# Kernel tuning notes

Hardware: AMD Instinct MI355X
Metric: run time of the kernel (lower is better)

Reference implementation:

```python
import jax, jax.numpy as jnp
import numpy as np
import math

EMBED = 1024
FF = 4096
HEADS = 16
HEAD = EMBED // HEADS
EPS = 1e-5


def new_gelu(x):
    c = math.sqrt(2.0 / math.pi)
    return 0.5 * x * (1.0 + jnp.tanh(c * (x + 0.044715 * x ** 3)))


def layer_norm(x, g, b):
    mu = jnp.mean(x, axis=-1, keepdims=True)
    var = jnp.var(x, axis=-1, keepdims=True)
    return (x - mu) * jax.lax.rsqrt(var + EPS) * g + b


def setup_inputs() -> dict:
    key = jax.random.key(0)
    ks = jax.random.split(key, 16)
    s = 0.02
    d = {
        'x': jax.random.normal(ks[0], (2, 2048, EMBED), jnp.float32),
        'Wq': jax.random.normal(ks[1], (EMBED, EMBED)) * s,
        'bq': jnp.zeros((EMBED,)),
        'Wk': jax.random.normal(ks[2], (EMBED, EMBED)) * s,
        'bk': jnp.zeros((EMBED,)),
        'Wv': jax.random.normal(ks[3], (EMBED, EMBED)) * s,
        'bv': jnp.zeros((EMBED,)),
        'Wp': jax.random.normal(ks[4], (EMBED, EMBED)) * s,
        'bp': jnp.zeros((EMBED,)),
        'W1': jax.random.normal(ks[5], (EMBED, FF)) * s,
        'b1': jnp.zeros((FF,)),
        'W2': jax.random.normal(ks[6], (FF, EMBED)) * s,
        'b2': jnp.zeros((EMBED,)),
        'g1': jnp.ones((EMBED,)), 'be1': jnp.zeros((EMBED,)),
        'g2': jnp.ones((EMBED,)), 'be2': jnp.zeros((EMBED,)),
    }
    return d


def reference(x, Wq, bq, Wk, bk, Wv, bv, Wp, bp, W1, b1, W2, b2, g1, be1, g2, be2):
    B, S, D = x.shape
    h = layer_norm(x, g1, be1)
    # project and split heads: [B,S,D] -> [B,H,S,Hd]
    def heads(y):
        return y.reshape(B, S, HEADS, HEAD).transpose(0, 2, 1, 3)
    Q = heads(h @ Wq + bq)
    K = heads(h @ Wk + bk)
    V = heads(h @ Wv + bv)
    att = jnp.einsum('bhqd,bhkd->bhqk', Q, K) / math.sqrt(HEAD)
    att = jax.nn.softmax(att, axis=-1)
    out = jnp.einsum('bhqk,bhkd->bhqd', att, V)
    out = out.transpose(0, 2, 1, 3).reshape(B, S, D)
    x = x + (out @ Wp + bp)  # dropout p=0 / eval -> identity
    h2 = layer_norm(x, g2, be2)
    x = x + (new_gelu(h2 @ W1 + b1) @ W2 + b2)
    return x
```

## Files before the change

### kernel.cpp

```cpp
#include <hip/hip_runtime.h>
#include <cstdint>


typedef __attribute__((ext_vector_type(8))) short short8;
typedef __attribute__((ext_vector_type(4))) float f32x4;

__device__ __forceinline__ float bf2f(unsigned short u) {
    union { unsigned int i; float f; } v; v.i = ((unsigned int)u) << 16; return v.f;
}
__device__ __forceinline__ unsigned short f2bf(float f) {
    union { float f; unsigned int i; } v; v.f = f;
    unsigned int u = v.i;
    u += 0x7fff + ((u >> 16) & 1);
    return (unsigned short)(u >> 16);
}
__device__ __forceinline__ float gelu_f(float x) {
    float u = 0.7978845608028654f * (x + 0.044715f * x * x * x);
    float t = 1.f - 2.f / (__expf(2.f * u) + 1.f);
    return 0.5f * x * (1.f + t);
}
__device__ __forceinline__ void async16(const unsigned short* gp, unsigned short* lp) {
    __builtin_amdgcn_global_load_lds(
        (__attribute__((address_space(1))) void*)(gp),
        (__attribute__((address_space(3))) void*)(lp),
        16, 0, 0);
}

__device__ __forceinline__ void ln_dev(
    const float* __restrict__ x, const float* __restrict__ g,
    const float* __restrict__ b, unsigned short* __restrict__ o,
    int row, float* red)
{
    const int tid = threadIdx.x;
    const float4 v = ((const float4*)(x + (size_t)row * 1024))[tid];
    float f0 = v.x, f1 = v.y, f2 = v.z, f3 = v.w;
    float sum = f0 + f1 + f2 + f3;
    float sq  = f0 * f0 + f1 * f1 + f2 * f2 + f3 * f3;
    for (int off = 1; off < 64; off <<= 1) {
        sum += __shfl_xor(sum, off);
        sq  += __shfl_xor(sq,  off);
    }
    int wv = tid >> 6, ln = tid & 63;
    if (ln == 0) { red[wv] = sum; red[4 + wv] = sq; }
    __syncthreads();
    sum = red[0] + red[1] + red[2] + red[3];
    sq  = red[4] + red[5] + red[6] + red[7];
    float mu  = sum * (1.0f / 1024.0f);
    float var = sq  * (1.0f / 1024.0f) - mu * mu;
    float rsd = rsqrtf(fmaxf(var, 0.f) + 1e-5f);
    const float4 gg = ((const float4*)g)[tid];
    const float4 bb = ((const float4*)b)[tid];
    unsigned short* orow = o + (size_t)row * 1024;
    orow[4 * tid + 0] = f2bf((f0 - mu) * rsd * gg.x + bb.x);
    orow[4 * tid + 1] = f2bf((f1 - mu) * rsd * gg.y + bb.y);
    orow[4 * tid + 2] = f2bf((f2 - mu) * rsd * gg.z + bb.z);
    orow[4 * tid + 3] = f2bf((f3 - mu) * rsd * gg.w + bb.w);
}

__device__ __forceinline__ void transpose_dev(
    const float* __restrict__ in, unsigned short* __restrict__ out,
    int R, int C, int inStride, int bx, int by, unsigned short* tile )
{
    const int tx = threadIdx.x & 15, ty = threadIdx.x >> 4;
    const int c0 = bx * 64, r0 = by * 64;
#pragma unroll
    for (int i = 0; i < 4; ++i) {
        int r = ty + 16 * i;
        float4 v = *(const float4*)(in + (size_t)(r0 + r) * inStride + c0 + tx * 4);
        tile[r * 70 + tx * 4 + 0] = f2bf(v.x);
        tile[r * 70 + tx * 4 + 1] = f2bf(v.y);
        tile[r * 70 + tx * 4 + 2] = f2bf(v.z);
        tile[r * 70 + tx * 4 + 3] = f2bf(v.w);
    }
    __syncthreads();
#pragma unroll
    for (int i = 0; i < 4; ++i) {
        int c = ty * 4 + i;
        ushort4 o;
        o.x = tile[(tx * 4 + 0) * 70 + c];
        o.y = tile[(tx * 4 + 1) * 70 + c];
        o.z = tile[(tx * 4 + 2) * 70 + c];
        o.w = tile[(tx * 4 + 3) * 70 + c];
        *(ushort4*)(out + (size_t)(c0 + c) * R + r0 + tx * 4) = o;
    }
}

__global__ __launch_bounds__(256) void ln_k(
    const float* __restrict__ x, const float* __restrict__ g,
    const float* __restrict__ b, unsigned short* __restrict__ o)
{
    __shared__ float red[8];
    ln_dev(x, g, b, o, blockIdx.x, red);
}
__global__ __launch_bounds__(256) void transpose_f2b(
    const float* __restrict__ in, unsigned short* __restrict__ out,
    int R, int C, int inStride)
{
    __shared__ unsigned short tile[64 * 70];
    transpose_dev(in, out, R, C, inStride, blockIdx.x, blockIdx.y, tile);
}
__global__ __launch_bounds__(256) void bcat_k(
    const float* __restrict__ a, const float* __restrict__ b,
    const float* __restrict__ c, float* __restrict__ dst)
{
    int i = blockIdx.x * 256 + threadIdx.x;
    float v = (i < 1024) ? a[i] : (i < 2048) ? b[i - 1024] : c[i - 2048];
    dst[i] = v;
}

__global__ __launch_bounds__(256) void prep1_k(
    const float* __restrict__ x,
    const float* __restrict__ g1, const float* __restrict__ be1,
    const float* __restrict__ Wq, const float* __restrict__ Wk,
    const float* __restrict__ Wv,
    const float* __restrict__ bq, const float* __restrict__ bk,
    const float* __restrict__ bv,
    unsigned short* __restrict__ hb,
    unsigned short* __restrict__ WTqkv,
    float* __restrict__ bcat)
{
    __shared__ unsigned short smem[64 * 70];
    const int b = blockIdx.x;
    if (b < 4096) {
        ln_dev(x, g1, be1, hb, b, (float*)smem);
    } else if (b < 4096 + 768) {
        int t = b - 4096;
        int w = t >> 8;
        int tt = t & 255;
        const float* W = (w == 0) ? Wq : (w == 1) ? Wk : Wv;
        transpose_dev(W, WTqkv + (size_t)w * 1024 * 1024,
                      1024, 1024, 1024, tt & 15, tt >> 4, smem);
    } else {
        int i = (b - 4096 - 768) * 256 + threadIdx.x;
        float v = (i < 1024) ? bq[i] : (i < 2048) ? bk[i - 1024] : bv[i - 2048];
        bcat[i] = v;
    }
}

__global__ __launch_bounds__(256) void prep2_k(
    const float* __restrict__ x1,
    const float* __restrict__ g2, const float* __restrict__ be2,
    const float* __restrict__ W1, const float* __restrict__ W2,
    unsigned short* __restrict__ h2,
    unsigned short* __restrict__ WT1,
    unsigned short* __restrict__ WT2)
{
    __shared__ unsigned short smem[64 * 70];
    const int b = blockIdx.x;
    if (b < 4096) {
        ln_dev(x1, g2, be2, h2, b, (float*)smem);
    } else if (b < 4096 + 1024) {
        int t = b - 4096;
        transpose_dev(W1, WT1, 1024, 4096, 4096, t & 63, t >> 6, smem);
    } else {
        int t = b - 4096 - 1024;
        transpose_dev(W2, WT2, 4096, 1024, 1024, t & 15, t >> 4, smem);
    }
}

__global__ __launch_bounds__(256) void vt_k(
    const unsigned short* __restrict__ src, int stride,
    unsigned short* __restrict__ Vt)
{
    __shared__ unsigned short tile[64][70];
    const int tx = threadIdx.x & 15, ty = threadIdx.x >> 4;
    const int t0 = blockIdx.x * 64;
    const int bh = blockIdx.y;
    const int bo = (bh >> 4) * 2048;
    const int ho = (bh & 15) * 64;
    const unsigned short* s = src + (size_t)bo * stride + ho;
#pragma unroll
    for (int i = 0; i < 4; ++i) {
        int r = ty + 16 * i;
        ushort4 v = *(const ushort4*)(s + (size_t)(t0 + r) * stride + tx * 4);
        tile[r][tx * 4 + 0] = v.x;
        tile[r][tx * 4 + 1] = v.y;
        tile[r][tx * 4 + 2] = v.z;
        tile[r][tx * 4 + 3] = v.w;
    }
    __syncthreads();
    unsigned short* dst = Vt + (size_t)bh * 64 * 2048;
#pragma unroll
    for (int i = 0; i < 4; ++i) {
        int d = ty * 4 + i;
#pragma unroll
        for (int c = 0; c < 4; ++c) {
            int t = tx * 4 + c;
            int sg = (t & 15) * 4 + (t >> 4);
            dst[(size_t)d * 2048 + t0 + sg] = tile[t][d];
        }
    }
}

__global__ __launch_bounds__(256, 2) void gemm_bt(
    const unsigned short* __restrict__ A,
    const unsigned short* __restrict__ Bt,
    const float* __restrict__ bias,
    const float* __restrict__ res,
    void* __restrict__ C,
    int M, int N, int K, int ldb, int dogelu, int out32)
{
    __shared__ unsigned short sA[2 * 128 * 32];
    __shared__ unsigned short sB[2 * 128 * 32];
    const int tid  = threadIdx.x;
    const int wave = tid >> 6;
    const int lane = tid & 63;
    const int quad = lane >> 4;
    const int l15  = lane & 15;
    const int bm = blockIdx.y * 128;
    const int bn = blockIdx.x * 128;
    const int wM = (wave >> 1) * 64;
    const int wN = (wave & 1) * 64;

    f32x4 acc[4][4];
#pragma unroll
    for (int i = 0; i < 4; ++i)
#pragma unroll
        for (int j = 0; j < 4; ++j)
            acc[i][j] = (f32x4){0.f, 0.f, 0.f, 0.f};

    const int rowS = tid >> 2;
    const int kcS  = (tid & 3) * 8;
    const unsigned short* gA  = A  + (size_t)(bm + rowS) * K + kcS;
    const unsigned short* gA2 = gA + (size_t)64 * K;
    const unsigned short* gB  = Bt + (size_t)(bn + rowS) * ldb + kcS;
    const unsigned short* gB2 = gB + (size_t)64 * ldb;
    unsigned short* lA  = sA + tid * 8;
    unsigned short* lA2 = lA + 64 * 32;
    unsigned short* lB  = sB + tid * 8;
    unsigned short* lB2 = lB + 64 * 32;

    for (int k0 = 0; k0 < K; k0 += 64) {
        __syncthreads();
        async16(gA + k0,       lA);
        async16(gA2 + k0,      lA2);
        async16(gA + k0 + 32,  lA + 4096);
        async16(gA2 + k0 + 32, lA2 + 4096);
        async16(gB + k0,       lB);
        async16(gB2 + k0,      lB2);
        async16(gB + k0 + 32,  lB + 4096);
        async16(gB2 + k0 + 32, lB2 + 4096);
        __syncthreads();

#pragma unroll
        for (int p = 0; p < 2; ++p) {
            short8 aF[4], bF[4];
#pragma unroll
            for (int mi = 0; mi < 4; ++mi)
                aF[mi] = *(const short8*)(sA + p * 4096 + (wM + mi * 16 + l15) * 32 + quad * 8);
#pragma unroll
            for (int ni = 0; ni < 4; ++ni)
                bF[ni] = *(const short8*)(sB + p * 4096 + (wN + ni * 16 + l15) * 32 + quad * 8);
#pragma unroll
            for (int mi = 0; mi < 4; ++mi)
#pragma unroll
                for (int ni = 0; ni < 4; ++ni)
                    acc[mi][ni] = __builtin_amdgcn_mfma_f32_16x16x32_bf16(
                        aF[mi], bF[ni], acc[mi][ni], 0, 0, 0);
        }
    }

#pragma unroll
    for (int ni = 0; ni < 4; ++ni) {
        int col = bn + wN + ni * 16 + l15;
        float bv = bias ? bias[col] : 0.f;
#pragma unroll
        for (int mi = 0; mi < 4; ++mi) {
            int row = bm + wM + mi * 16 + quad * 4;
#pragma unroll
            for (int r = 0; r < 4; ++r) {
                float v = acc[mi][ni][r] + bv;
                if (dogelu) v = gelu_f(v);
                size_t idx = (size_t)(row + r) * N + col;
                if (res) v += res[idx];
                if (out32) ((float*)C)[idx] = v;
                else       ((unsigned short*)C)[idx] = f2bf(v);
            }
        }
    }
}

__global__ __launch_bounds__(256, 2) void gemm_bt64(
    const unsigned short* __restrict__ A,
    const unsigned short* __restrict__ Bt,
    const float* __restrict__ bias,
    const float* __restrict__ res,
    void* __restrict__ C,
    int M, int N, int K, int ldb, int dogelu, int out32)
{
    __shared__ unsigned short sA[2 * 128 * 32];
    __shared__ unsigned short sB[2 * 64 * 32];
    const int tid  = threadIdx.x;
    const int wave = tid >> 6;
    const int lane = tid & 63;
    const int quad = lane >> 4;
    const int l15  = lane & 15;
    const int bm = blockIdx.y * 128;
    const int bn = blockIdx.x * 64;
    const int wM = wave * 32;

    f32x4 acc[2][4];
#pragma unroll
    for (int i = 0; i < 2; ++i)
#pragma unroll
        for (int j = 0; j < 4; ++j)
            acc[i][j] = (f32x4){0.f, 0.f, 0.f, 0.f};

    const int rowS = tid >> 2;
    const int kcS  = (tid & 3) * 8;
    const unsigned short* gA  = A  + (size_t)(bm + rowS) * K + kcS;
    const unsigned short* gA2 = gA + (size_t)64 * K;
    const unsigned short* gB  = Bt + (size_t)(bn + rowS) * ldb + kcS;
    unsigned short* lA  = sA + tid * 8;
    unsigned short* lA2 = lA + 64 * 32;
    unsigned short* lB  = sB + tid * 8;

    for (int k0 = 0; k0 < K; k0 += 64) {
        __syncthreads();
        async16(gA + k0,       lA);
        async16(gA2 + k0,      lA2);
        async16(gA + k0 + 32,  lA + 4096);
        async16(gA2 + k0 + 32, lA2 + 4096);
        async16(gB + k0,       lB);
        async16(gB + k0 + 32,  lB + 2048);
        __syncthreads();

#pragma unroll
        for (int p = 0; p < 2; ++p) {
            short8 aF[2], bF[4];
#pragma unroll
            for (int mi = 0; mi < 2; ++mi)
                aF[mi] = *(const short8*)(sA + p * 4096 + (wM + mi * 16 + l15) * 32 + quad * 8);
#pragma unroll
            for (int ni = 0; ni < 4; ++ni)
                bF[ni] = *(const short8*)(sB + p * 2048 + (ni * 16 + l15) * 32 + quad * 8);
#pragma unroll
            for (int mi = 0; mi < 2; ++mi)
#pragma unroll
                for (int ni = 0; ni < 4; ++ni)
                    acc[mi][ni] = __builtin_amdgcn_mfma_f32_16x16x32_bf16(
                        aF[mi], bF[ni], acc[mi][ni], 0, 0, 0);
        }
    }

#pragma unroll
    for (int ni = 0; ni < 4; ++ni) {
        int col = bn + ni * 16 + l15;
        float bv = bias ? bias[col] : 0.f;
#pragma unroll
        for (int mi = 0; mi < 2; ++mi) {
            int row = bm + wM + mi * 16 + quad * 4;
#pragma unroll
            for (int r = 0; r < 4; ++r) {
                float v = acc[mi][ni][r] + bv;
                if (dogelu) v = gelu_f(v);
                size_t idx = (size_t)(row + r) * N + col;
                if (res) v += res[idx];
                if (out32) ((float*)C)[idx] = v;
                else       ((unsigned short*)C)[idx] = f2bf(v);
            }
        }
    }
}

__global__ __launch_bounds__(256, 1) void attn_k(
    const unsigned short* __restrict__ Q,
    const unsigned short* __restrict__ K,
    const unsigned short* __restrict__ Vt,
    unsigned short* __restrict__ O, int qs)
{
    __shared__ unsigned short sK[2][64 * 88];
    __shared__ unsigned short sV[2][64 * 88];
    __shared__ unsigned short sP[4][64 * 88];

    const int tid  = threadIdx.x;
    const int wave = tid >> 6;
    const int lane = tid & 63;
    const int quad = lane >> 4;
    const int l15  = lane & 15;
    const int qb = blockIdx.x * 256;
    const int bh = blockIdx.y;
    const int bo = (bh >> 4) * 2048;
    const int ho = (bh & 15) * 64;

    const unsigned short* Qb  = Q  + (size_t)bo * qs + ho;
    const unsigned short* Kb  = K  + (size_t)bo * qs + ho;
    const unsigned short* Vtb = Vt + (size_t)bh * 64 * 2048;
    unsigned short* sPw = sP[wave];

    short8 qF[2][4];
#pragma unroll
    for (int ks = 0; ks < 2; ++ks)
#pragma unroll
        for (int mi = 0; mi < 4; ++mi)
            qF[ks][mi] = *(const short8*)(Qb +
                (size_t)(qb + wave * 64 + mi * 16 + l15) * qs + ks * 32 + quad * 8);

    short8 onesF;
#pragma unroll
    for (int j = 0; j < 8; ++j) onesF[j] = (short)0x3F80;

    f32x4 accO[4][4];
    f32x4 accL[4];
#pragma unroll
    for (int mi = 0; mi < 4; ++mi) {
        accL[mi] = (f32x4){0.f, 0.f, 0.f, 0.f};
#pragma unroll
        for (int nd = 0; nd < 4; ++nd) accO[mi][nd] = (f32x4){0.f, 0.f, 0.f, 0.f};
    }

    const int rowS = tid >> 3;
    const int dcS  = (tid & 7) * 8;

    short8 kr[2], vr[2];
#pragma unroll
    for (int r = 0; r < 2; ++r) {
        kr[r] = *(const short8*)(Kb + (size_t)(r * 32 + rowS) * qs + dcS);
        vr[r] = *(const short8*)(Vtb + (size_t)(r * 32 + rowS) * 2048 + dcS);
    }
#pragma unroll
    for (int r = 0; r < 2; ++r) {
        *(short8*)(&sK[0][(r * 32 + rowS) * 88 + dcS]) = kr[r];
        *(short8*)(&sV[0][(r * 32 + rowS) * 88 + dcS]) = vr[r];
    }
#pragma unroll
    for (int r = 0; r < 2; ++r) {
        kr[r] = *(const short8*)(Kb + (size_t)(64 + r * 32 + rowS) * qs + dcS);
        vr[r] = *(const short8*)(Vtb + (size_t)(r * 32 + rowS) * 2048 + 64 + dcS);
    }

    for (int kt = 0; kt < 2048; kt += 64) {
        const int buf = (kt >> 6) & 1;
        __syncthreads();

        short8 bK[2][4];
#pragma unroll
        for (int ks = 0; ks < 2; ++ks)
#pragma unroll
            for (int ni = 0; ni < 4; ++ni)
                bK[ks][ni] = *(const short8*)(&sK[buf][(ni * 16 + l15) * 88 + ks * 32 + quad * 8]);

#pragma unroll
        for (int mi = 0; mi < 4; ++mi) {
            f32x4 s0 = (f32x4){0.f, 0.f, 0.f, 0.f};
            f32x4 s1 = s0, s2 = s0, s3 = s0;
#pragma unroll
            for (int ks = 0; ks < 2; ++ks) {
                s0 = __builtin_amdgcn_mfma_f32_16x16x32_bf16(qF[ks][mi], bK[ks][0], s0, 0, 0, 0);
                s1 = __builtin_amdgcn_mfma_f32_16x16x32_bf16(qF[ks][mi], bK[ks][1], s1, 0, 0, 0);
                s2 = __builtin_amdgcn_mfma_f32_16x16x32_bf16(qF[ks][mi], bK[ks][2], s2, 0, 0, 0);
                s3 = __builtin_amdgcn_mfma_f32_16x16x32_bf16(qF[ks][mi], bK[ks][3], s3, 0, 0, 0);
            }
#pragma unroll
            for (int r = 0; r < 4; ++r) {
                float p0 = __expf(s0[r] * 0.125f);
                float p1 = __expf(s1[r] * 0.125f);
                float p2 = __expf(s2[r] * 0.125f);
                float p3 = __expf(s3[r] * 0.125f);
                unsigned int w0, w1;
                asm("v_cvt_pk_bf16_f32 %0, %1, %2" : "=v"(w0) : "v"(p0), "v"(p1));
                asm("v_cvt_pk_bf16_f32 %0, %1, %2" : "=v"(w1) : "v"(p2), "v"(p3));
                uint2 w; w.x = w0; w.y = w1;
                *(uint2*)(&sPw[(mi * 16 + quad * 4 + r) * 88 + l15 * 4]) = w;
            }
        }

        if (kt + 64 < 2048) {
            const int nb = buf ^ 1;
#pragma unroll
            for (int r = 0; r < 2; ++r) {
                *(short8*)(&sK[nb][(r * 32 + rowS) * 88 + dcS]) = kr[r];
                *(short8*)(&sV[nb][(r * 32 + rowS) * 88 + dcS]) = vr[r];
            }
            if (kt + 128 < 2048) {
#pragma unroll
                for (int r = 0; r < 2; ++r) {
                    kr[r] = *(const short8*)(Kb + (size_t)(kt + 128 + r * 32 + rowS) * qs + dcS);
                    vr[r] = *(const short8*)(Vtb + (size_t)(r * 32 + rowS) * 2048 + kt + 128 + dcS);
                }
            }
        }

        short8 bV[2][4];
#pragma unroll
        for (int ks = 0; ks < 2; ++ks)
#pragma unroll
            for (int nd = 0; nd < 4; ++nd)
                bV[ks][nd] = *(const short8*)(&sV[buf][(nd * 16 + l15) * 88 + ks * 32 + quad * 8]);

        __builtin_amdgcn_s_setprio(1);
#pragma unroll
        for (int mi = 0; mi < 4; ++mi) {
            short8 aP0 = *(const short8*)(&sPw[(mi * 16 + l15) * 88 + quad * 8]);
            short8 aP1 = *(const short8*)(&sPw[(mi * 16 + l15) * 88 + 32 + quad * 8]);
#pragma unroll
            for (int nd = 0; nd < 4; ++nd) {
                accO[mi][nd] = __builtin_amdgcn_mfma_f32_16x16x32_bf16(
                    aP0, bV[0][nd], accO[mi][nd], 0, 0, 0);
                accO[mi][nd] = __builtin_amdgcn_mfma_f32_16x16x32_bf16(
                    aP1, bV[1][nd], accO[mi][nd], 0, 0, 0);
            }
            accL[mi] = __builtin_amdgcn_mfma_f32_16x16x32_bf16(aP0, onesF, accL[mi], 0, 0, 0);
            accL[mi] = __builtin_amdgcn_mfma_f32_16x16x32_bf16(aP1, onesF, accL[mi], 0, 0, 0);
        }
        __builtin_amdgcn_s_setprio(0);
    }

#pragma unroll
    for (int mi = 0; mi < 4; ++mi)
#pragma unroll
        for (int r = 0; r < 4; ++r) {
            int row = qb + wave * 64 + mi * 16 + quad * 4 + r;
            float inv = 1.f / accL[mi][r];
#pragma unroll
            for (int nd = 0; nd < 4; ++nd)
                O[(size_t)(bo + row) * 1024 + ho + nd * 16 + l15] =
                    f2bf(accO[mi][nd][r] * inv);
        }
}

extern "C" void kernel_launch(void* const* d_in, const int* in_sizes, int n_in,
                              void* d_out, int out_size, void* d_ws, size_t ws_size,
                              hipStream_t stream)
{
    (void)in_sizes; (void)n_in; (void)out_size;
    const float* x   = (const float*)d_in[0];
    const float* Wq  = (const float*)d_in[1];
    const float* bq  = (const float*)d_in[2];
    const float* Wk  = (const float*)d_in[3];
    const float* bk  = (const float*)d_in[4];
    const float* Wv  = (const float*)d_in[5];
    const float* bv  = (const float*)d_in[6];
    const float* Wp  = (const float*)d_in[7];
    const float* bp  = (const float*)d_in[8];
    const float* W1  = (const float*)d_in[9];
    const float* b1  = (const float*)d_in[10];
    const float* W2  = (const float*)d_in[11];
    const float* b2  = (const float*)d_in[12];
    const float* g1  = (const float*)d_in[13];
    const float* be1 = (const float*)d_in[14];
    const float* g2  = (const float*)d_in[15];
    const float* be2 = (const float*)d_in[16];
    float* out = (float*)d_out;

    char* ws = (char*)d_ws;
    char* dob = (char*)d_out;
    const size_t MB = 1024 * 1024;

    if (ws_size >= 40 * MB) {
        unsigned short* hb    = (unsigned short*)dob;
        unsigned short* WTqkv = (unsigned short*)(dob + 8 * MB);
        float*          bcat  = (float*)(dob + 14 * MB);
        unsigned short* QKV   = (unsigned short*)ws;
        unsigned short* att   = (unsigned short*)(ws + 24 * MB);
        unsigned short* Vt    = (unsigned short*)(ws + 32 * MB);
        unsigned short* WTp   = (unsigned short*)(ws + 32 * MB);
        unsigned short* h2    = (unsigned short*)ws;
        unsigned short* WT1   = (unsigned short*)(ws + 8 * MB);
        unsigned short* WT2   = (unsigned short*)(ws + 16 * MB);
        unsigned short* act   = (unsigned short*)(ws + 24 * MB);

        prep1_k<<<4096 + 768 + 12, 256, 0, stream>>>(
            x, g1, be1, Wq, Wk, Wv, bq, bk, bv, hb, WTqkv, bcat);
        gemm_bt<<<dim3(24, 32), 256, 0, stream>>>(hb, WTqkv, bcat, nullptr, QKV,
                                                  4096, 3072, 1024, 1024, 0, 0);
        vt_k<<<dim3(32, 32), 256, 0, stream>>>(QKV + 2048, 3072, Vt);
        attn_k<<<dim3(8, 32), 256, 0, stream>>>(QKV, QKV + 1024, Vt, att, 3072);
        transpose_f2b<<<dim3(16, 16), 256, 0, stream>>>(Wp, WTp, 1024, 1024, 1024);
        gemm_bt64<<<dim3(16, 32), 256, 0, stream>>>(att, WTp, bp, x, out,
                                                    4096, 1024, 1024, 1024, 0, 1);
        prep2_k<<<4096 + 2048, 256, 0, stream>>>(out, g2, be2, W1, W2, h2, WT1, WT2);
        for (int c = 0; c < 2; ++c) {
            gemm_bt<<<dim3(16, 32), 256, 0, stream>>>(h2, WT1 + (size_t)c * 2048 * 1024,
                                                      b1 + c * 2048, nullptr, act,
                                                      4096, 2048, 1024, 1024, 1, 0);
            gemm_bt64<<<dim3(16, 32), 256, 0, stream>>>(act, WT2 + (size_t)c * 2048,
                                                        c == 0 ? b2 : nullptr, out, out,
                                                        4096, 1024, 2048, 4096, 0, 1);
        }
    } else {
        unsigned short* Qw  = (unsigned short*)(ws);
        unsigned short* Kw  = (unsigned short*)(ws + 8 * MB);
        unsigned short* Vw  = (unsigned short*)(ws + 16 * MB);
        unsigned short* hb  = (unsigned short*)dob;
        unsigned short* WTq = (unsigned short*)(dob + 8 * MB);
        unsigned short* VtF = (unsigned short*)(dob + 8 * MB);
        unsigned short* att = Qw;
        unsigned short* WTb = Kw;
        unsigned short* h2  = Vw;
        unsigned short* act = Qw;

        ln_k<<<4096, 256, 0, stream>>>(x, g1, be1, hb);
        transpose_f2b<<<dim3(16, 16), 256, 0, stream>>>(Wq, WTq, 1024, 1024, 1024);
        gemm_bt<<<dim3(8, 32), 256, 0, stream>>>(hb, WTq, bq, nullptr, Qw, 4096, 1024, 1024, 1024, 0, 0);
        transpose_f2b<<<dim3(16, 16), 256, 0, stream>>>(Wk, WTq, 1024, 1024, 1024);
        gemm_bt<<<dim3(8, 32), 256, 0, stream>>>(hb, WTq, bk, nullptr, Kw, 4096, 1024, 1024, 1024, 0, 0);
        transpose_f2b<<<dim3(16, 16), 256, 0, stream>>>(Wv, WTq, 1024, 1024, 1024);
        gemm_bt<<<dim3(8, 32), 256, 0, stream>>>(hb, WTq, bv, nullptr, Vw, 4096, 1024, 1024, 1024, 0, 0);
        vt_k<<<dim3(32, 32), 256, 0, stream>>>(Vw, 1024, VtF);
        attn_k<<<dim3(8, 32), 256, 0, stream>>>(Qw, Kw, VtF, att, 1024);
        transpose_f2b<<<dim3(16, 16), 256, 0, stream>>>(Wp, WTb, 1024, 1024, 1024);
        gemm_bt64<<<dim3(16, 32), 256, 0, stream>>>(att, WTb, bp, x, out, 4096, 1024, 1024, 1024, 0, 1);
        ln_k<<<4096, 256, 0, stream>>>(out, g2, be2, h2);
        for (int c = 0; c < 4; ++c) {
            transpose_f2b<<<dim3(16, 16), 256, 0, stream>>>(W1 + c * 1024, WTb, 1024, 1024, 4096);
            gemm_bt64<<<dim3(16, 32), 256, 0, stream>>>(h2, WTb, b1 + c * 1024, nullptr, act,
                                                        4096, 1024, 1024, 1024, 1, 0);
            unsigned short* WT2c = WTb + 1024 * 1024;
            transpose_f2b<<<dim3(16, 16), 256, 0, stream>>>(W2 + (size_t)c * 1024 * 1024, WT2c,
                                                            1024, 1024, 1024);
            gemm_bt64<<<dim3(16, 32), 256, 0, stream>>>(act, WT2c, c == 0 ? b2 : nullptr,
                                                        out, out, 4096, 1024, 1024, 1024, 0, 1);
        }
    }
}
```

Measured before the change: 399.3 us.

## Split attention keys across wave pairs, fold softmax scale into Wq, vectorize V transpose

Attention now runs 8 waves per block: each group of four waves shares a query tile, and the two halves split the QK^T key columns and the PV reduction dimension. Partial outputs are then combined through shared memory. The 1/sqrt(d)*log2(e) scale is folded into Wq and bq at transpose time, so the softmax uses exp2 directly with no per-element multiply. The V transpose kernel writes ushort4 vectors, and gemm_bt's launch bound rises to 3 blocks per SM. The attention kernel adds an extra barrier per tile and a final cross-wave reduction, and occupancy depends on the larger shared-memory footprint.

```diff
diff --git a/kernel.cpp b/kernel.cpp
--- a/kernel.cpp
+++ b/kernel.cpp
@@ -4,6 +4,8 @@
 
 typedef __attribute__((ext_vector_type(8))) short short8;
 typedef __attribute__((ext_vector_type(4))) float f32x4;
+
+#define QSCL 0.18033688011112042f
 
 __device__ __forceinline__ float bf2f(unsigned short u) {
     union { unsigned int i; float f; } v; v.i = ((unsigned int)u) << 16; return v.f;
@@ -59,7 +61,8 @@
 
 __device__ __forceinline__ void transpose_dev(
     const float* __restrict__ in, unsigned short* __restrict__ out,
-    int R, int C, int inStride, int bx, int by, unsigned short* tile )
+    int R, int C, int inStride, int bx, int by, unsigned short* tile ,
+    float scale)
 {
     const int tx = threadIdx.x & 15, ty = threadIdx.x >> 4;
     const int c0 = bx * 64, r0 = by * 64;
@@ -67,10 +70,10 @@
     for (int i = 0; i < 4; ++i) {
         int r = ty + 16 * i;
         float4 v = *(const float4*)(in + (size_t)(r0 + r) * inStride + c0 + tx * 4);
-        tile[r * 70 + tx * 4 + 0] = f2bf(v.x);
-        tile[r * 70 + tx * 4 + 1] = f2bf(v.y);
-        tile[r * 70 + tx * 4 + 2] = f2bf(v.z);
-        tile[r * 70 + tx * 4 + 3] = f2bf(v.w);
+        tile[r * 70 + tx * 4 + 0] = f2bf(v.x * scale);
+        tile[r * 70 + tx * 4 + 1] = f2bf(v.y * scale);
+        tile[r * 70 + tx * 4 + 2] = f2bf(v.z * scale);
+        tile[r * 70 + tx * 4 + 3] = f2bf(v.w * scale);
     }
     __syncthreads();
 #pragma unroll
@@ -94,18 +97,10 @@
 }
 __global__ __launch_bounds__(256) void transpose_f2b(
     const float* __restrict__ in, unsigned short* __restrict__ out,
-    int R, int C, int inStride)
+    int R, int C, int inStride, float scale)
 {
     __shared__ unsigned short tile[64 * 70];
-    transpose_dev(in, out, R, C, inStride, blockIdx.x, blockIdx.y, tile);
-}
-__global__ __launch_bounds__(256) void bcat_k(
-    const float* __restrict__ a, const float* __restrict__ b,
-    const float* __restrict__ c, float* __restrict__ dst)
-{
-    int i = blockIdx.x * 256 + threadIdx.x;
-    float v = (i < 1024) ? a[i] : (i < 2048) ? b[i - 1024] : c[i - 2048];
-    dst[i] = v;
+    transpose_dev(in, out, R, C, inStride, blockIdx.x, blockIdx.y, tile, scale);
 }
 
 __global__ __launch_bounds__(256) void prep1_k(
@@ -129,10 +124,11 @@
         int tt = t & 255;
         const float* W = (w == 0) ? Wq : (w == 1) ? Wk : Wv;
         transpose_dev(W, WTqkv + (size_t)w * 1024 * 1024,
-                      1024, 1024, 1024, tt & 15, tt >> 4, smem);
+                      1024, 1024, 1024, tt & 15, tt >> 4, smem,
+                      (w == 0) ? QSCL : 1.f);
     } else {
         int i = (b - 4096 - 768) * 256 + threadIdx.x;
-        float v = (i < 1024) ? bq[i] : (i < 2048) ? bk[i - 1024] : bv[i - 2048];
+        float v = (i < 1024) ? bq[i] * QSCL : (i < 2048) ? bk[i - 1024] : bv[i - 2048];
         bcat[i] = v;
     }
 }
@@ -151,10 +147,10 @@
         ln_dev(x1, g2, be2, h2, b, (float*)smem);
     } else if (b < 4096 + 1024) {
         int t = b - 4096;
-        transpose_dev(W1, WT1, 1024, 4096, 4096, t & 63, t >> 6, smem);
+        transpose_dev(W1, WT1, 1024, 4096, 4096, t & 63, t >> 6, smem, 1.f);
     } else {
         int t = b - 4096 - 1024;
-        transpose_dev(W2, WT2, 4096, 1024, 1024, t & 15, t >> 4, smem);
+        transpose_dev(W2, WT2, 4096, 1024, 1024, t & 15, t >> 4, smem, 1.f);
     }
 }
 
@@ -183,22 +179,23 @@
 #pragma unroll
     for (int i = 0; i < 4; ++i) {
         int d = ty * 4 + i;
-#pragma unroll
-        for (int c = 0; c < 4; ++c) {
-            int t = tx * 4 + c;
-            int sg = (t & 15) * 4 + (t >> 4);
-            dst[(size_t)d * 2048 + t0 + sg] = tile[t][d];
-        }
-    }
-}
-
-__global__ __launch_bounds__(256, 2) void gemm_bt(
+        int u = tx;
+        ushort4 o;
+        o.x = tile[u +  0][d];
+        o.y = tile[u + 16][d];
+        o.z = tile[u + 32][d];
+        o.w = tile[u + 48][d];
+        *(ushort4*)(dst + (size_t)d * 2048 + t0 + u * 4) = o;
+    }
+}
+
+__global__ __launch_bounds__(256, 3) void gemm_bt(
     const unsigned short* __restrict__ A,
     const unsigned short* __restrict__ Bt,
     const float* __restrict__ bias,
     const float* __restrict__ res,
     void* __restrict__ C,
-    int M, int N, int K, int ldb, int dogelu, int out32)
+    int M, int N, int K, int ldb, int dogelu, int out32, float bscale)
 {
     __shared__ unsigned short sA[2 * 128 * 32];
     __shared__ unsigned short sB[2 * 128 * 32];
@@ -263,7 +260,7 @@
 #pragma unroll
     for (int ni = 0; ni < 4; ++ni) {
         int col = bn + wN + ni * 16 + l15;
-        float bv = bias ? bias[col] : 0.f;
+        float bv = bias ? bias[col] * bscale : 0.f;
 #pragma unroll
         for (int mi = 0; mi < 4; ++mi) {
             int row = bm + wM + mi * 16 + quad * 4;
@@ -363,18 +360,21 @@
     }
 }
 
-__global__ __launch_bounds__(256, 1) void attn_k(
+__global__ __launch_bounds__(512, 2) void attn_k(
     const unsigned short* __restrict__ Q,
     const unsigned short* __restrict__ K,
     const unsigned short* __restrict__ Vt,
     unsigned short* __restrict__ O, int qs)
 {
-    __shared__ unsigned short sK[2][64 * 88];
-    __shared__ unsigned short sV[2][64 * 88];
-    __shared__ unsigned short sP[4][64 * 88];
+    __shared__ unsigned short smem[45056];
+    unsigned short* sK = smem;
+    unsigned short* sV = smem + 2 * 5632;
+    unsigned short* sP = smem + 4 * 5632;
 
     const int tid  = threadIdx.x;
     const int wave = tid >> 6;
+    const int g    = wave & 3;
+    const int h    = wave >> 2;
     const int lane = tid & 63;
     const int quad = lane >> 4;
     const int l15  = lane & 15;
@@ -386,7 +386,8 @@
     const unsigned short* Qb  = Q  + (size_t)bo * qs + ho;
     const unsigned short* Kb  = K  + (size_t)bo * qs + ho;
     const unsigned short* Vtb = Vt + (size_t)bh * 64 * 2048;
-    unsigned short* sPw = sP[wave];
+    unsigned short* sPg = sP + g * 5632;
+    const int ni0 = 2 * h;
 
     short8 qF[2][4];
 #pragma unroll
@@ -394,7 +395,7 @@
 #pragma unroll
         for (int mi = 0; mi < 4; ++mi)
             qF[ks][mi] = *(const short8*)(Qb +
-                (size_t)(qb + wave * 64 + mi * 16 + l15) * qs + ks * 32 + quad * 8);
+                (size_t)(qb + g * 64 + mi * 16 + l15) * qs + ks * 32 + quad * 8);
 
     short8 onesF;
 #pragma unroll
@@ -412,111 +413,111 @@
     const int rowS = tid >> 3;
     const int dcS  = (tid & 7) * 8;
 
-    short8 kr[2], vr[2];
-#pragma unroll
-    for (int r = 0; r < 2; ++r) {
-        kr[r] = *(const short8*)(Kb + (size_t)(r * 32 + rowS) * qs + dcS);
-        vr[r] = *(const short8*)(Vtb + (size_t)(r * 32 + rowS) * 2048 + dcS);
-    }
-#pragma unroll
-    for (int r = 0; r < 2; ++r) {
-        *(short8*)(&sK[0][(r * 32 + rowS) * 88 + dcS]) = kr[r];
-        *(short8*)(&sV[0][(r * 32 + rowS) * 88 + dcS]) = vr[r];
-    }
-#pragma unroll
-    for (int r = 0; r < 2; ++r) {
-        kr[r] = *(const short8*)(Kb + (size_t)(64 + r * 32 + rowS) * qs + dcS);
-        vr[r] = *(const short8*)(Vtb + (size_t)(r * 32 + rowS) * 2048 + 64 + dcS);
-    }
+    short8 kr, vr;
+    kr = *(const short8*)(Kb + (size_t)rowS * qs + dcS);
+    vr = *(const short8*)(Vtb + (size_t)rowS * 2048 + dcS);
+    *(short8*)(sK + rowS * 88 + dcS) = kr;
+    *(short8*)(sV + rowS * 88 + dcS) = vr;
+    kr = *(const short8*)(Kb + (size_t)(64 + rowS) * qs + dcS);
+    vr = *(const short8*)(Vtb + (size_t)rowS * 2048 + 64 + dcS);
 
     for (int kt = 0; kt < 2048; kt += 64) {
         const int buf = (kt >> 6) & 1;
         __syncthreads();
 
-        short8 bK[2][4];
+        short8 bK[2][2];
 #pragma unroll
         for (int ks = 0; ks < 2; ++ks)
 #pragma unroll
-            for (int ni = 0; ni < 4; ++ni)
-                bK[ks][ni] = *(const short8*)(&sK[buf][(ni * 16 + l15) * 88 + ks * 32 + quad * 8]);
+            for (int nj = 0; nj < 2; ++nj)
+                bK[ks][nj] = *(const short8*)(sK + buf * 5632 +
+                    ((ni0 + nj) * 16 + l15) * 88 + ks * 32 + quad * 8);
 
 #pragma unroll
         for (int mi = 0; mi < 4; ++mi) {
             f32x4 s0 = (f32x4){0.f, 0.f, 0.f, 0.f};
-            f32x4 s1 = s0, s2 = s0, s3 = s0;
+            f32x4 s1 = s0;
 #pragma unroll
             for (int ks = 0; ks < 2; ++ks) {
                 s0 = __builtin_amdgcn_mfma_f32_16x16x32_bf16(qF[ks][mi], bK[ks][0], s0, 0, 0, 0);
                 s1 = __builtin_amdgcn_mfma_f32_16x16x32_bf16(qF[ks][mi], bK[ks][1], s1, 0, 0, 0);
-                s2 = __builtin_amdgcn_mfma_f32_16x16x32_bf16(qF[ks][mi], bK[ks][2], s2, 0, 0, 0);
-                s3 = __builtin_amdgcn_mfma_f32_16x16x32_bf16(qF[ks][mi], bK[ks][3], s3, 0, 0, 0);
             }
 #pragma unroll
             for (int r = 0; r < 4; ++r) {
-                float p0 = __expf(s0[r] * 0.125f);
-                float p1 = __expf(s1[r] * 0.125f);
-                float p2 = __expf(s2[r] * 0.125f);
-                float p3 = __expf(s3[r] * 0.125f);
-                unsigned int w0, w1;
-                asm("v_cvt_pk_bf16_f32 %0, %1, %2" : "=v"(w0) : "v"(p0), "v"(p1));
-                asm("v_cvt_pk_bf16_f32 %0, %1, %2" : "=v"(w1) : "v"(p2), "v"(p3));
-                uint2 w; w.x = w0; w.y = w1;
-                *(uint2*)(&sPw[(mi * 16 + quad * 4 + r) * 88 + l15 * 4]) = w;
+                float p0 = __builtin_amdgcn_exp2f(s0[r]);
+                float p1 = __builtin_amdgcn_exp2f(s1[r]);
+                unsigned int w;
+                asm("v_cvt_pk_bf16_f32 %0, %1, %2" : "=v"(w) : "v"(p0), "v"(p1));
+                *(unsigned int*)(sPg + (mi * 16 + quad * 4 + r) * 88 + l15 * 4 + ni0) = w;
             }
         }
 
+        __syncthreads();
+
+        short8 aP[4], bV[4];
+#pragma unroll
+        for (int nd = 0; nd < 4; ++nd)
+            bV[nd] = *(const short8*)(sV + buf * 5632 + (nd * 16 + l15) * 88 + h * 32 + quad * 8);
+#pragma unroll
+        for (int mi = 0; mi < 4; ++mi)
+            aP[mi] = *(const short8*)(sPg + (mi * 16 + l15) * 88 + h * 32 + quad * 8);
+
         if (kt + 64 < 2048) {
-            const int nb = buf ^ 1;
-#pragma unroll
-            for (int r = 0; r < 2; ++r) {
-                *(short8*)(&sK[nb][(r * 32 + rowS) * 88 + dcS]) = kr[r];
-                *(short8*)(&sV[nb][(r * 32 + rowS) * 88 + dcS]) = vr[r];
+            *(short8*)(sK + (buf ^ 1) * 5632 + rowS * 88 + dcS) = kr;
+            *(short8*)(sV + (buf ^ 1) * 5632 + rowS * 88 + dcS) = vr;
+            if (kt + 128 < 2048) {
+                kr = *(const short8*)(Kb + (size_t)(kt + 128 + rowS) * qs + dcS);
+                vr = *(const short8*)(Vtb + (size_t)rowS * 2048 + kt + 128 + dcS);
             }
-            if (kt + 128 < 2048) {
-#pragma unroll
-                for (int r = 0; r < 2; ++r) {
-                    kr[r] = *(const short8*)(Kb + (size_t)(kt + 128 + r * 32 + rowS) * qs + dcS);
-                    vr[r] = *(const short8*)(Vtb + (size_t)(r * 32 + rowS) * 2048 + kt + 128 + dcS);
-                }
+        }
+
+        __builtin_amdgcn_s_setprio(1);
+#pragma unroll
+        for (int mi = 0; mi < 4; ++mi) {
+#pragma unroll
+            for (int nd = 0; nd < 4; ++nd)
+                accO[mi][nd] = __builtin_amdgcn_mfma_f32_16x16x32_bf16(
+                    aP[mi], bV[nd], accO[mi][nd], 0, 0, 0);
+            accL[mi] = __builtin_amdgcn_mfma_f32_16x16x32_bf16(
+                aP[mi], onesF, accL[mi], 0, 0, 0);
+        }
+        __builtin_amdgcn_s_setprio(0);
+    }
+
+    __syncthreads();
+    float* scr = (float*)smem;
+    float* po = scr + (size_t)(g * 64 + lane) * 68;
+    float* pl = scr + 17408 + (size_t)(g * 64 + lane) * 20;
+    if (h == 1) {
+#pragma unroll
+        for (int mi = 0; mi < 4; ++mi) {
+#pragma unroll
+            for (int nd = 0; nd < 4; ++nd)
+                *(f32x4*)(po + mi * 16 + nd * 4) = accO[mi][nd];
+            *(f32x4*)(pl + mi * 4) = accL[mi];
+        }
+    }
+    __syncthreads();
+    if (h == 0) {
+#pragma unroll
+        for (int mi = 0; mi < 4; ++mi) {
+            accL[mi] += *(const f32x4*)(pl + mi * 4);
+#pragma unroll
+            for (int nd = 0; nd < 4; ++nd)
+                accO[mi][nd] += *(const f32x4*)(po + mi * 16 + nd * 4);
+        }
+#pragma unroll
+        for (int mi = 0; mi < 4; ++mi)
+#pragma unroll
+            for (int r = 0; r < 4; ++r) {
+                int row = qb + g * 64 + mi * 16 + quad * 4 + r;
+                float inv = 1.f / accL[mi][r];
+#pragma unroll
+                for (int nd = 0; nd < 4; ++nd)
+                    O[(size_t)(bo + row) * 1024 + ho + nd * 16 + l15] =
+                        f2bf(accO[mi][nd][r] * inv);
             }
-        }
-
-        short8 bV[2][4];
-#pragma unroll
-        for (int ks = 0; ks < 2; ++ks)
-#pragma unroll
-            for (int nd = 0; nd < 4; ++nd)
-                bV[ks][nd] = *(const short8*)(&sV[buf][(nd * 16 + l15) * 88 + ks * 32 + quad * 8]);
-
-        __builtin_amdgcn_s_setprio(1);
-#pragma unroll
-        for (int mi = 0; mi < 4; ++mi) {
-            short8 aP0 = *(const short8*)(&sPw[(mi * 16 + l15) * 88 + quad * 8]);
-            short8 aP1 = *(const short8*)(&sPw[(mi * 16 + l15) * 88 + 32 + quad * 8]);
-#pragma unroll
-            for (int nd = 0; nd < 4; ++nd) {
-                accO[mi][nd] = __builtin_amdgcn_mfma_f32_16x16x32_bf16(
-                    aP0, bV[0][nd], accO[mi][nd], 0, 0, 0);
-                accO[mi][nd] = __builtin_amdgcn_mfma_f32_16x16x32_bf16(
-                    aP1, bV[1][nd], accO[mi][nd], 0, 0, 0);
-            }
-            accL[mi] = __builtin_amdgcn_mfma_f32_16x16x32_bf16(aP0, onesF, accL[mi], 0, 0, 0);
-            accL[mi] = __builtin_amdgcn_mfma_f32_16x16x32_bf16(aP1, onesF, accL[mi], 0, 0, 0);
-        }
-        __builtin_amdgcn_s_setprio(0);
-    }
-
-#pragma unroll
-    for (int mi = 0; mi < 4; ++mi)
-#pragma unroll
-        for (int r = 0; r < 4; ++r) {
-            int row = qb + wave * 64 + mi * 16 + quad * 4 + r;
-            float inv = 1.f / accL[mi][r];
-#pragma unroll
-            for (int nd = 0; nd < 4; ++nd)
-                O[(size_t)(bo + row) * 1024 + ho + nd * 16 + l15] =
-                    f2bf(accO[mi][nd][r] * inv);
-        }
+    }
 }
 
 extern "C" void kernel_launch(void* const* d_in, const int* in_sizes, int n_in,
@@ -563,17 +564,17 @@
         prep1_k<<<4096 + 768 + 12, 256, 0, stream>>>(
             x, g1, be1, Wq, Wk, Wv, bq, bk, bv, hb, WTqkv, bcat);
         gemm_bt<<<dim3(24, 32), 256, 0, stream>>>(hb, WTqkv, bcat, nullptr, QKV,
-                                                  4096, 3072, 1024, 1024, 0, 0);
+                                                  4096, 3072, 1024, 1024, 0, 0, 1.f);
         vt_k<<<dim3(32, 32), 256, 0, stream>>>(QKV + 2048, 3072, Vt);
-        attn_k<<<dim3(8, 32), 256, 0, stream>>>(QKV, QKV + 1024, Vt, att, 3072);
-        transpose_f2b<<<dim3(16, 16), 256, 0, stream>>>(Wp, WTp, 1024, 1024, 1024);
+        attn_k<<<dim3(8, 32), 512, 0, stream>>>(QKV, QKV + 1024, Vt, att, 3072);
+        transpose_f2b<<<dim3(16, 16), 256, 0, stream>>>(Wp, WTp, 1024, 1024, 1024, 1.f);
         gemm_bt64<<<dim3(16, 32), 256, 0, stream>>>(att, WTp, bp, x, out,
                                                     4096, 1024, 1024, 1024, 0, 1);
         prep2_k<<<4096 + 2048, 256, 0, stream>>>(out, g2, be2, W1, W2, h2, WT1, WT2);
         for (int c = 0; c < 2; ++c) {
             gemm_bt<<<dim3(16, 32), 256, 0, stream>>>(h2, WT1 + (size_t)c * 2048 * 1024,
                                                       b1 + c * 2048, nullptr, act,
-                                                      4096, 2048, 1024, 1024, 1, 0);
+                                                      4096, 2048, 1024, 1024, 1, 0, 1.f);
             gemm_bt64<<<dim3(16, 32), 256, 0, stream>>>(act, WT2 + (size_t)c * 2048,
                                                         c == 0 ? b2 : nullptr, out, out,
                                                         4096, 1024, 2048, 4096, 0, 1);
@@ -591,24 +592,24 @@
         unsigned short* act = Qw;
 
         ln_k<<<4096, 256, 0, stream>>>(x, g1, be1, hb);
-        transpose_f2b<<<dim3(16, 16), 256, 0, stream>>>(Wq, WTq, 1024, 1024, 1024);
-        gemm_bt<<<dim3(8, 32), 256, 0, stream>>>(hb, WTq, bq, nullptr, Qw, 4096, 1024, 1024, 1024, 0, 0);
-        transpose_f2b<<<dim3(16, 16), 256, 0, stream>>>(Wk, WTq, 1024, 1024, 1024);
-        gemm_bt<<<dim3(8, 32), 256, 0, stream>>>(hb, WTq, bk, nullptr, Kw, 4096, 1024, 1024, 1024, 0, 0);
-        transpose_f2b<<<dim3(16, 16), 256, 0, stream>>>(Wv, WTq, 1024, 1024, 1024);
-        gemm_bt<<<dim3(8, 32), 256, 0, stream>>>(hb, WTq, bv, nullptr, Vw, 4096, 1024, 1024, 1024, 0, 0);
+        transpose_f2b<<<dim3(16, 16), 256, 0, stream>>>(Wq, WTq, 1024, 1024, 1024, QSCL);
+        gemm_bt<<<dim3(8, 32), 256, 0, stream>>>(hb, WTq, bq, nullptr, Qw, 4096, 1024, 1024, 1024, 0, 0, QSCL);
+        transpose_f2b<<<dim3(16, 16), 256, 0, stream>>>(Wk, WTq, 1024, 1024, 1024, 1.f);
+        gemm_bt<<<dim3(8, 32), 256, 0, stream>>>(hb, WTq, bk, nullptr, Kw, 4096, 1024, 1024, 1024, 0, 0, 1.f);
+        transpose_f2b<<<dim3(16, 16), 256, 0, stream>>>(Wv, WTq, 1024, 1024, 1024, 1.f);
+        gemm_bt<<<dim3(8, 32), 256, 0, stream>>>(hb, WTq, bv, nullptr, Vw, 4096, 1024, 1024, 1024, 0, 0, 1.f);
         vt_k<<<dim3(32, 32), 256, 0, stream>>>(Vw, 1024, VtF);
-        attn_k<<<dim3(8, 32), 256, 0, stream>>>(Qw, Kw, VtF, att, 1024);
-        transpose_f2b<<<dim3(16, 16), 256, 0, stream>>>(Wp, WTb, 1024, 1024, 1024);
+        attn_k<<<dim3(8, 32), 512, 0, stream>>>(Qw, Kw, VtF, att, 1024);
+        transpose_f2b<<<dim3(16, 16), 256, 0, stream>>>(Wp, WTb, 1024, 1024, 1024, 1.f);
         gemm_bt64<<<dim3(16, 32), 256, 0, stream>>>(att, WTb, bp, x, out, 4096, 1024, 1024, 1024, 0, 1);
         ln_k<<<4096, 256, 0, stream>>>(out, g2, be2, h2);
         for (int c = 0; c < 4; ++c) {
-            transpose_f2b<<<dim3(16, 16), 256, 0, stream>>>(W1 + c * 1024, WTb, 1024, 1024, 4096);
+            transpose_f2b<<<dim3(16, 16), 256, 0, stream>>>(W1 + c * 1024, WTb, 1024, 1024, 4096, 1.f);
             gemm_bt64<<<dim3(16, 32), 256, 0, stream>>>(h2, WTb, b1 + c * 1024, nullptr, act,
                                                         4096, 1024, 1024, 1024, 1, 0);
             unsigned short* WT2c = WTb + 1024 * 1024;
             transpose_f2b<<<dim3(16, 16), 256, 0, stream>>>(W2 + (size_t)c * 1024 * 1024, WT2c,
-                                                            1024, 1024, 1024);
+                                                            1024, 1024, 1024, 1.f);
             gemm_bt64<<<dim3(16, 32), 256, 0, stream>>>(act, WT2c, c == 0 ? b2 : nullptr,
                                                         out, out, 4096, 1024, 1024, 1024, 0, 1);
         }
```

After: 378.0 us. -5.3%, faster.
